# Kernel optimization log

Measured on AMD Instinct MI355X. Metric: run time of the kernel, lower is better.

Reference implementation:

```python
import jax, jax.numpy as jnp
import numpy as np

D_MODEL = 1024
N_HEADS = 16
D_HEAD = D_MODEL // N_HEADS


def setup_inputs() -> dict:
    key = jax.random.key(0)
    kx, kq, kk, kv, ko = jax.random.split(key, 5)
    s = 1.0 / np.sqrt(D_MODEL)
    return {
        "x": jax.random.normal(kx, (2, 2048, D_MODEL), dtype=jnp.float32),
        "Wq": jax.random.normal(kq, (D_MODEL, D_MODEL), dtype=jnp.float32) * s,
        "Wk": jax.random.normal(kk, (D_MODEL, D_MODEL), dtype=jnp.float32) * s,
        "Wv": jax.random.normal(kv, (D_MODEL, D_MODEL), dtype=jnp.float32) * s,
        "Wo": jax.random.normal(ko, (D_MODEL, D_MODEL), dtype=jnp.float32) * s,
    }


def reference(x, Wq, Wk, Wv, Wo):
    B, T, _ = x.shape
    def split_heads(t):  # [B,T,D] -> [B,H,T,d]
        return t.reshape(B, T, N_HEADS, D_HEAD).transpose(0, 2, 1, 3)
    q = split_heads(x @ Wq)
    k = split_heads(x @ Wk)
    v = split_heads(x @ Wv)
    scale = jnp.asarray(D_HEAD, x.dtype) ** -0.5
    att = jnp.einsum("bhqd,bhkd->bhqk", q, k) * scale
    mask = jnp.tril(jnp.ones((T, T), dtype=x.dtype))  # 1 on/below diag
    att = att + (1.0 - mask)[None, None] * jnp.asarray(-1e9, x.dtype)
    w = jax.nn.softmax(att, axis=-1)
    y = jnp.einsum("bhqk,bhkd->bhqd", w, v)
    y = y.transpose(0, 2, 1, 3).reshape(B, T, D_MODEL)
    return y @ Wo
```

## Files before the change

### kernel.cpp

```cpp
#include <hip/hip_runtime.h>

#define DM 1024
#define NH 16
#define TT 2048
#define BB 2
#define NTOK (BB*TT)
#define DQKV 3072

typedef __attribute__((ext_vector_type(8))) short bf16x8;
typedef __attribute__((ext_vector_type(4))) float f32x4;
typedef __attribute__((ext_vector_type(4))) int  int4v;

static __device__ __forceinline__ short f2b(float f) {
  union { float f; unsigned u; } v; v.f = f;
  unsigned r = v.u + 0x7FFFu + ((v.u >> 16) & 1u);
  return (short)(r >> 16);
}

__global__ __launch_bounds__(256) void k_convert(const float* __restrict__ in,
                                                 short* __restrict__ out, int n) {
  int i = (blockIdx.x * 256 + threadIdx.x) * 8;
  if (i >= n) return;
  float4 a = *(const float4*)(in + i);
  float4 b = *(const float4*)(in + i + 4);
  bf16x8 o;
  o[0]=f2b(a.x); o[1]=f2b(a.y); o[2]=f2b(a.z); o[3]=f2b(a.w);
  o[4]=f2b(b.x); o[5]=f2b(b.y); o[6]=f2b(b.z); o[7]=f2b(b.w);
  *(bf16x8*)(out + i) = o;
}

__global__ __launch_bounds__(256) void k_transpose_w4(const float* __restrict__ Wq,
                                                      const float* __restrict__ Wk,
                                                      const float* __restrict__ Wv,
                                                      const float* __restrict__ Wo,
                                                      short* __restrict__ WqkvT,
                                                      short* __restrict__ WoT) {
  __shared__ short t[64][72];
  const int z = blockIdx.z;
  const float* W = (z == 0) ? Wq : (z == 1) ? Wk : (z == 2) ? Wv : Wo;
  short* Wt = (z < 3) ? WqkvT : WoT;
  const int row0 = (z < 3) ? z * 1024 : 0;
  int tid = threadIdx.x;
  int n0 = blockIdx.x * 64, k0 = blockIdx.y * 64;
  #pragma unroll
  for (int i = 0; i < 4; i++) {
    int id = tid + 256 * i;
    int r = id >> 4;
    int c = id & 15;
    float4 v = *(const float4*)(W + (size_t)(k0 + r) * DM + n0 + c * 4);
    t[c*4+0][r] = f2b(v.x);
    t[c*4+1][r] = f2b(v.y);
    t[c*4+2][r] = f2b(v.z);
    t[c*4+3][r] = f2b(v.w);
  }
  __syncthreads();
  #pragma unroll
  for (int i = 0; i < 2; i++) {
    int id = tid + 256 * i;
    int r = id >> 3;
    int c = id & 7;
    bf16x8 o = *(const bf16x8*)&t[r][c * 8];
    *(bf16x8*)(Wt + (size_t)(row0 + n0 + r) * DM + k0 + c * 8) = o;
  }
}

__global__ __launch_bounds__(256) void k_transpose_v(const short* __restrict__ V,
                                                     short* __restrict__ Vt) {
  __shared__ short t[64][72];
  int tid = threadIdx.x;
  int bh = blockIdx.y;
  int b = bh >> 4, h = bh & 15;
  int t0 = blockIdx.x * 64;
  #pragma unroll
  for (int i = 0; i < 2; i++) {
    int id = tid + 256 * i;
    int r = id >> 3;
    int c = id & 7;
    int kp = ((r & 15) << 2) | (r >> 4);
    bf16x8 v = *(const bf16x8*)(V + (size_t)(b * TT + t0 + r) * DQKV + h * 64 + c * 8);
    #pragma unroll
    for (int e = 0; e < 8; e++) t[c * 8 + e][kp] = v[e];
  }
  __syncthreads();
  #pragma unroll
  for (int i = 0; i < 2; i++) {
    int id = tid + 256 * i;
    int r = id >> 3;
    int c = id & 7;
    bf16x8 o = *(const bf16x8*)&t[r][c * 8];
    *(bf16x8*)(Vt + (size_t)(bh * 64 + r) * TT + t0 + c * 8) = o;
  }
}

template<int OUT_BF16, int BN>
__global__ __launch_bounds__(256) void k_gemm_lds(const short* __restrict__ A,
                                                  const short* __restrict__ Bt,
                                                  void* __restrict__ C,
                                                  int M, int N, int K,
                                                  int qcols, float qscale) {
  __shared__ short As[2][128 * 64];
  __shared__ short Bs[2][BN * 64];
  constexpr int NI = BN / 32;
  const int tid = threadIdx.x;
  const int lane = tid & 63, w = tid >> 6;
  const int wm = w >> 1, wn = w & 1;
  const int l15 = lane & 15, g = lane >> 4;
  const int nx = N / BN;
  const int cx = nx >> 3;
  const int bid = blockIdx.x;
  const int xcd = bid & 7, k_ = bid >> 3;
  const int bx = xcd * cx + (k_ % cx), by = k_ / cx;
  const int m0 = by * 128, n0 = bx * BN;
  const int srow = lane >> 3;
  const int scol = ((lane & 7) ^ srow) * 8;
  const int rsw = l15 & 7;

  auto stage = [&](int buf, int k0) {
    #pragma unroll
    for (int i = 0; i < 4; i++) {
      int rbase = w * 32 + i * 8;
      __builtin_amdgcn_global_load_lds(
        (const __attribute__((address_space(1))) void*)(A + (size_t)(m0 + rbase + srow) * K + k0 + scol),
        (__attribute__((address_space(3))) void*)&As[buf][rbase * 64],
        16, 0, 0);
    }
    #pragma unroll
    for (int i = 0; i < BN / 32; i++) {
      int rbase = w * (BN / 4) + i * 8;
      __builtin_amdgcn_global_load_lds(
        (const __attribute__((address_space(1))) void*)(Bt + (size_t)(n0 + rbase + srow) * K + k0 + scol),
        (__attribute__((address_space(3))) void*)&Bs[buf][rbase * 64],
        16, 0, 0);
    }
  };

  f32x4 acc[4][NI] = {};
  stage(0, 0);
  __syncthreads();
  const int nt = K / 64;
  for (int t = 0; t < nt; t++) {
    const int cur = t & 1;
    if (t + 1 < nt) stage(cur ^ 1, (t + 1) * 64);
    #pragma unroll
    for (int kk = 0; kk < 64; kk += 32) {
      bf16x8 af[4], bfr[NI];
      #pragma unroll
      for (int mi = 0; mi < 4; mi++)
        af[mi] = *(const bf16x8*)&As[cur][(wm * 64 + mi * 16 + l15) * 64 + ((((kk >> 3) + g) ^ rsw) << 3)];
      #pragma unroll
      for (int ni = 0; ni < NI; ni++)
        bfr[ni] = *(const bf16x8*)&Bs[cur][(wn * (BN / 2) + ni * 16 + l15) * 64 + ((((kk >> 3) + g) ^ rsw) << 3)];
      #pragma unroll
      for (int mi = 0; mi < 4; mi++)
        #pragma unroll
        for (int ni = 0; ni < NI; ni++)
          acc[mi][ni] = __builtin_amdgcn_mfma_f32_16x16x32_bf16(af[mi], bfr[ni], acc[mi][ni], 0, 0, 0);
    }
    __syncthreads();
  }

  if (OUT_BF16) {
    short* Cs = &As[0][0];
    #pragma unroll
    for (int mi = 0; mi < 4; mi++) {
      #pragma unroll
      for (int ni = 0; ni < NI; ni++) {
        #pragma unroll
        for (int j = 0; j < 4; j++) {
          int row = wm * 64 + mi * 16 + g * 4 + j;
          int col = wn * (BN / 2) + ni * 16 + l15;
          float v = acc[mi][ni][j];
          if (n0 + col < qcols) v *= qscale;
          Cs[row * BN + col] = f2b(v);
        }
      }
    }
    __syncthreads();
    constexpr int UNITS = 128 * BN / 8;
    #pragma unroll
    for (int u = tid; u < UNITS; u += 256) {
      int row = u / (BN / 8), ch = u % (BN / 8);
      bf16x8 vv = *(const bf16x8*)&Cs[row * BN + ch * 8];
      *(bf16x8*)((short*)C + (size_t)(m0 + row) * N + n0 + ch * 8) = vv;
    }
  } else {
    #pragma unroll
    for (int mi = 0; mi < 4; mi++) {
      #pragma unroll
      for (int ni = 0; ni < NI; ni++) {
        #pragma unroll
        for (int j = 0; j < 4; j++) {
          int row = m0 + wm * 64 + mi * 16 + g * 4 + j;
          int col = n0 + wn * (BN / 2) + ni * 16 + l15;
          ((float*)C)[(size_t)row * N + col] = acc[mi][ni][j];
        }
      }
    }
  }
}

__global__ __launch_bounds__(256) void k_attn(const short* __restrict__ Qkv,
                                              const short* __restrict__ Vt,
                                              short* __restrict__ Y) {
  __shared__ short Ks[2][64 * 64];
  __shared__ short Vs[2][64 * 64];
  __shared__ short Ps[4][16 * 64];
  const int tid = threadIdx.x;
  const int lane = tid & 63, w = tid >> 6;
  const int l15 = lane & 15, g = lane >> 4;
  const int bx = blockIdx.x;
  const int xcd = bx & 7, idx = bx >> 3;
  const int bh = xcd * 4 + (idx & 3);
  const int qt = 31 - (idx >> 2);
  const int b = bh >> 4, h = bh & 15;
  const int q0 = qt * 64;
  const int nkt = qt + 1;
  const short* Qb = Qkv;
  const short* Kb = Qkv + DM;
  short* PsW = Ps[w];
  const int rsw = l15 & 7;

  const bf16x8 vones = {0x3F80, 0x3F80, 0x3F80, 0x3F80, 0x3F80, 0x3F80, 0x3F80, 0x3F80};

  auto stage = [&](int buf, int kt) {
    #pragma unroll
    for (int i = 0; i < 2; i++) {
      int id = tid + 256 * i;
      int r = id >> 3;
      int cl = (id ^ r) & 7;
      __builtin_amdgcn_global_load_lds(
        (const __attribute__((address_space(1))) void*)(Kb + (size_t)(b * TT + kt * 64 + r) * DQKV + h * 64 + cl * 8),
        (__attribute__((address_space(3))) void*)&Ks[buf][(w * 64 + 256 * i) * 8],
        16, 0, 0);
      __builtin_amdgcn_global_load_lds(
        (const __attribute__((address_space(1))) void*)(Vt + (size_t)(bh * 64 + r) * TT + kt * 64 + cl * 8),
        (__attribute__((address_space(3))) void*)&Vs[buf][(w * 64 + 256 * i) * 8],
        16, 0, 0);
    }
  };

  bf16x8 aq[2];
  #pragma unroll
  for (int kc = 0; kc < 2; kc++)
    aq[kc] = *(const bf16x8*)(Qb + (size_t)(b * TT + q0 + w * 16 + l15) * DQKV + h * 64 + kc * 32 + 8 * g);

  f32x4 accO[4] = {};
  f32x4 accL = {};
  float m2[4];
  #pragma unroll
  for (int j = 0; j < 4; j++) m2[j] = -1e30f;

  stage(0, 0);
  __syncthreads();

  for (int kt = 0; kt < nkt; kt++) {
    const int cur = kt & 1;
    if (kt + 1 < nkt) stage(cur ^ 1, kt + 1);

    f32x4 accS[4] = {};
    __builtin_amdgcn_s_setprio(1);
    #pragma unroll
    for (int n = 0; n < 4; n++) {
      #pragma unroll
      for (int kc = 0; kc < 2; kc++) {
        bf16x8 bk = *(const bf16x8*)&Ks[cur][(n * 16 + l15) * 64 + (((kc * 4 + g) ^ rsw) << 3)];
        accS[n] = __builtin_amdgcn_mfma_f32_16x16x32_bf16(aq[kc], bk, accS[n], 0, 0, 0);
      }
    }
    __builtin_amdgcn_s_setprio(0);

    float tmaxp[4];
    #pragma unroll
    for (int j = 0; j < 4; j++) tmaxp[j] = -1e30f;
    const int qbase = q0 + w * 16 + g * 4;
    if (kt == qt) {
      #pragma unroll
      for (int n = 0; n < 4; n++) {
        int key = kt * 64 + n * 16 + l15;
        #pragma unroll
        for (int j = 0; j < 4; j++) {
          float s = accS[n][j];
          if (key > qbase + j) s = -1e30f;
          accS[n][j] = s;
          tmaxp[j] = fmaxf(tmaxp[j], s);
        }
      }
    } else {
      #pragma unroll
      for (int n = 0; n < 4; n++)
        #pragma unroll
        for (int j = 0; j < 4; j++)
          tmaxp[j] = fmaxf(tmaxp[j], accS[n][j]);
    }

    float dmax = fmaxf(fmaxf(tmaxp[0] - m2[0], tmaxp[1] - m2[1]),
                       fmaxf(tmaxp[2] - m2[2], tmaxp[3] - m2[3]));
    if (!__all(dmax <= 8.0f)) {
      #pragma unroll
      for (int j = 0; j < 4; j++) {
        float t = tmaxp[j];
        #pragma unroll
        for (int off = 1; off < 16; off <<= 1)
          t = fmaxf(t, __shfl_xor(t, off));
        float mnew = fmaxf(m2[j], t);
        float al = exp2f(m2[j] - mnew);
        m2[j] = mnew;
        accL[j] *= al;
        #pragma unroll
        for (int n2 = 0; n2 < 4; n2++) accO[n2][j] *= al;
      }
    }

    #pragma unroll
    for (int j = 0; j < 4; j++) {
      const int row = g * 4 + j;
      union { float f; unsigned u; } c0, c1, c2, c3;
      c0.f = exp2f(accS[0][j] - m2[j]);
      c1.f = exp2f(accS[1][j] - m2[j]);
      c2.f = exp2f(accS[2][j] - m2[j]);
      c3.f = exp2f(accS[3][j] - m2[j]);
      int2 pk;
      pk.x = (int)((c0.u >> 16) | (c1.u & 0xFFFF0000u));
      pk.y = (int)((c2.u >> 16) | (c3.u & 0xFFFF0000u));
      const int c8 = l15 ^ ((row & 7) << 1);
      *(int2*)&PsW[row * 64 + (c8 << 2)] = pk;
    }

    __builtin_amdgcn_s_setprio(1);
    #pragma unroll
    for (int kc = 0; kc < 2; kc++) {
      bf16x8 pa = *(const bf16x8*)&PsW[l15 * 64 + (((kc * 4 + g) ^ rsw) << 3)];
      #pragma unroll
      for (int n2 = 0; n2 < 4; n2++) {
        bf16x8 vb = *(const bf16x8*)&Vs[cur][(n2 * 16 + l15) * 64 + (((kc * 4 + g) ^ rsw) << 3)];
        accO[n2] = __builtin_amdgcn_mfma_f32_16x16x32_bf16(pa, vb, accO[n2], 0, 0, 0);
      }
      accL = __builtin_amdgcn_mfma_f32_16x16x32_bf16(pa, vones, accL, 0, 0, 0);
    }
    __builtin_amdgcn_s_setprio(0);

    __syncthreads();
  }

  float inv[4];
  #pragma unroll
  for (int j = 0; j < 4; j++) inv[j] = 1.0f / accL[j];
  #pragma unroll
  for (int n2 = 0; n2 < 4; n2++) {
    #pragma unroll
    for (int j = 0; j < 4; j++) {
      float v = accO[n2][j] * inv[j];
      PsW[(g * 4 + j) * 64 + n2 * 16 + l15] = f2b(v);
    }
  }
  const int orow = b * TT + q0 + w * 16;
  #pragma unroll
  for (int i = 0; i < 2; i++) {
    int unit = lane + 64 * i;
    int row = unit >> 3, ch = unit & 7;
    bf16x8 vv = *(const bf16x8*)&PsW[row * 64 + ch * 8];
    *(bf16x8*)(Y + (size_t)(orow + row) * DM + h * 64 + ch * 8) = vv;
  }
}

extern "C" void kernel_launch(void* const* d_in, const int* in_sizes, int n_in,
                              void* d_out, int out_size, void* d_ws, size_t ws_size,
                              hipStream_t stream) {
  const float* x  = (const float*)d_in[0];
  const float* Wq = (const float*)d_in[1];
  const float* Wk = (const float*)d_in[2];
  const float* Wv = (const float*)d_in[3];
  const float* Wo = (const float*)d_in[4];
  float* out = (float*)d_out;

  char* ws = (char*)d_ws;
  size_t off = 0;
  auto alloc = [&](size_t bytes) {
    char* p = ws + off;
    off += (bytes + 255) & ~(size_t)255;
    return p;
  };
  short* xb    = (short*)alloc((size_t)NTOK * DM * 2);
  short* WqkvT = (short*)alloc((size_t)DQKV * DM * 2);
  short* WoT   = (short*)alloc((size_t)DM * DM * 2);
  short* Qkv   = (short*)alloc((size_t)NTOK * DQKV * 2);
  short* Vt    = (short*)alloc((size_t)NTOK * DM * 2);
  short* Yb    = xb;
  if (off > ws_size) return;

  k_convert<<<(NTOK * DM) / (256 * 8), 256, 0, stream>>>(x, xb, NTOK * DM);
  k_transpose_w4<<<dim3(DM / 64, DM / 64, 4), 256, 0, stream>>>(Wq, Wk, Wv, Wo, WqkvT, WoT);

  const float QSC = 0.125f * 1.44269504088896f;
  k_gemm_lds<1, 64><<<dim3((DQKV / 64) * (NTOK / 128)), 256, 0, stream>>>(xb, WqkvT, Qkv, NTOK, DQKV, DM, DM, QSC);

  k_transpose_v<<<dim3(TT / 64, BB * NH), 256, 0, stream>>>(Qkv + 2048, Vt);
  k_attn<<<dim3(1024), 256, 0, stream>>>(Qkv, Vt, Yb);

  k_gemm_lds<0, 64><<<dim3((DM / 64) * (NTOK / 128)), 256, 0, stream>>>(Yb, WoT, out, NTOK, DM, DM, 0, 1.0f);
}
```

Measured before the change: 110.9 us.

## Compute S transposed so P feeds PV MFMA from registers, dropping LDS

```diff
diff --git a/kernel.cpp b/kernel.cpp
--- a/kernel.cpp
+++ b/kernel.cpp
@@ -76,7 +76,8 @@
     int id = tid + 256 * i;
     int r = id >> 3;
     int c = id & 7;
-    int kp = ((r & 15) << 2) | (r >> 4);
+    int n = r >> 4;
+    int kp = ((n >> 1) << 5) | (((r >> 2) & 3) << 3) | ((n & 1) << 2) | (r & 3);
     bf16x8 v = *(const bf16x8*)(V + (size_t)(b * TT + t0 + r) * DQKV + h * 64 + c * 8);
     #pragma unroll
     for (int e = 0; e < 8; e++) t[c * 8 + e][kp] = v[e];
@@ -204,7 +205,6 @@
                                               short* __restrict__ Y) {
   __shared__ short Ks[2][64 * 64];
   __shared__ short Vs[2][64 * 64];
-  __shared__ short Ps[4][16 * 64];
   const int tid = threadIdx.x;
   const int lane = tid & 63, w = tid >> 6;
   const int l15 = lane & 15, g = lane >> 4;
@@ -217,7 +217,6 @@
   const int nkt = qt + 1;
   const short* Qb = Qkv;
   const short* Kb = Qkv + DM;
-  short* PsW = Ps[w];
   const int rsw = l15 & 7;
 
   const bf16x8 vones = {0x3F80, 0x3F80, 0x3F80, 0x3F80, 0x3F80, 0x3F80, 0x3F80, 0x3F80};
@@ -246,9 +245,7 @@
 
   f32x4 accO[4] = {};
   f32x4 accL = {};
-  float m2[4];
-  #pragma unroll
-  for (int j = 0; j < 4; j++) m2[j] = -1e30f;
+  float m2 = -1e30f;
 
   stage(0, 0);
   __syncthreads();
@@ -264,72 +261,65 @@
       #pragma unroll
       for (int kc = 0; kc < 2; kc++) {
         bf16x8 bk = *(const bf16x8*)&Ks[cur][(n * 16 + l15) * 64 + (((kc * 4 + g) ^ rsw) << 3)];
-        accS[n] = __builtin_amdgcn_mfma_f32_16x16x32_bf16(aq[kc], bk, accS[n], 0, 0, 0);
+        accS[n] = __builtin_amdgcn_mfma_f32_16x16x32_bf16(bk, aq[kc], accS[n], 0, 0, 0);
       }
     }
     __builtin_amdgcn_s_setprio(0);
 
-    float tmaxp[4];
-    #pragma unroll
-    for (int j = 0; j < 4; j++) tmaxp[j] = -1e30f;
-    const int qbase = q0 + w * 16 + g * 4;
+    const int qg = q0 + w * 16 + l15;
     if (kt == qt) {
       #pragma unroll
       for (int n = 0; n < 4; n++) {
-        int key = kt * 64 + n * 16 + l15;
         #pragma unroll
         for (int j = 0; j < 4; j++) {
-          float s = accS[n][j];
-          if (key > qbase + j) s = -1e30f;
-          accS[n][j] = s;
-          tmaxp[j] = fmaxf(tmaxp[j], s);
+          int key = kt * 64 + n * 16 + g * 4 + j;
+          if (key > qg) accS[n][j] = -1e30f;
         }
       }
-    } else {
-      #pragma unroll
-      for (int n = 0; n < 4; n++)
-        #pragma unroll
-        for (int j = 0; j < 4; j++)
-          tmaxp[j] = fmaxf(tmaxp[j], accS[n][j]);
-    }
-
-    float dmax = fmaxf(fmaxf(tmaxp[0] - m2[0], tmaxp[1] - m2[1]),
-                       fmaxf(tmaxp[2] - m2[2], tmaxp[3] - m2[3]));
-    if (!__all(dmax <= 8.0f)) {
+    }
+    float tmax = -1e30f;
+    #pragma unroll
+    for (int n = 0; n < 4; n++)
+      #pragma unroll
+      for (int j = 0; j < 4; j++)
+        tmax = fmaxf(tmax, accS[n][j]);
+
+    if (!__all(tmax - m2 <= 8.0f)) {
+      float t1 = fmaxf(tmax, __shfl_xor(tmax, 16));
+      float full = fmaxf(t1, __shfl_xor(t1, 32));
+      float mnew = fmaxf(m2, full);
+      float al = exp2f(m2 - mnew);
+      m2 = mnew;
+      float alr[4];
+      #pragma unroll
+      for (int j = 0; j < 4; j++) alr[j] = __shfl(al, g * 4 + j);
+      #pragma unroll
+      for (int j = 0; j < 4; j++) accL[j] *= alr[j];
+      #pragma unroll
+      for (int n2 = 0; n2 < 4; n2++)
+        #pragma unroll
+        for (int j = 0; j < 4; j++) accO[n2][j] *= alr[j];
+    }
+
+    unsigned cu[4][4];
+    #pragma unroll
+    for (int n = 0; n < 4; n++)
       #pragma unroll
       for (int j = 0; j < 4; j++) {
-        float t = tmaxp[j];
-        #pragma unroll
-        for (int off = 1; off < 16; off <<= 1)
-          t = fmaxf(t, __shfl_xor(t, off));
-        float mnew = fmaxf(m2[j], t);
-        float al = exp2f(m2[j] - mnew);
-        m2[j] = mnew;
-        accL[j] *= al;
-        #pragma unroll
-        for (int n2 = 0; n2 < 4; n2++) accO[n2][j] *= al;
-      }
-    }
-
-    #pragma unroll
-    for (int j = 0; j < 4; j++) {
-      const int row = g * 4 + j;
-      union { float f; unsigned u; } c0, c1, c2, c3;
-      c0.f = exp2f(accS[0][j] - m2[j]);
-      c1.f = exp2f(accS[1][j] - m2[j]);
-      c2.f = exp2f(accS[2][j] - m2[j]);
-      c3.f = exp2f(accS[3][j] - m2[j]);
-      int2 pk;
-      pk.x = (int)((c0.u >> 16) | (c1.u & 0xFFFF0000u));
-      pk.y = (int)((c2.u >> 16) | (c3.u & 0xFFFF0000u));
-      const int c8 = l15 ^ ((row & 7) << 1);
-      *(int2*)&PsW[row * 64 + (c8 << 2)] = pk;
-    }
+        union { float f; unsigned u; } cv;
+        cv.f = exp2f(accS[n][j] - m2);
+        cu[n][j] = cv.u;
+      }
 
     __builtin_amdgcn_s_setprio(1);
     #pragma unroll
     for (int kc = 0; kc < 2; kc++) {
-      bf16x8 pa = *(const bf16x8*)&PsW[l15 * 64 + (((kc * 4 + g) ^ rsw) << 3)];
+      union { int4v i; bf16x8 h; } pu;
+      pu.i[0] = (int)((cu[2*kc+0][0] >> 16) | (cu[2*kc+0][1] & 0xFFFF0000u));
+      pu.i[1] = (int)((cu[2*kc+0][2] >> 16) | (cu[2*kc+0][3] & 0xFFFF0000u));
+      pu.i[2] = (int)((cu[2*kc+1][0] >> 16) | (cu[2*kc+1][1] & 0xFFFF0000u));
+      pu.i[3] = (int)((cu[2*kc+1][2] >> 16) | (cu[2*kc+1][3] & 0xFFFF0000u));
+      bf16x8 pa = pu.h;
       #pragma unroll
       for (int n2 = 0; n2 < 4; n2++) {
         bf16x8 vb = *(const bf16x8*)&Vs[cur][(n2 * 16 + l15) * 64 + (((kc * 4 + g) ^ rsw) << 3)];
@@ -345,12 +335,13 @@
   float inv[4];
   #pragma unroll
   for (int j = 0; j < 4; j++) inv[j] = 1.0f / accL[j];
+  short* Ys = &Ks[0][w * 1024];
   #pragma unroll
   for (int n2 = 0; n2 < 4; n2++) {
     #pragma unroll
     for (int j = 0; j < 4; j++) {
       float v = accO[n2][j] * inv[j];
-      PsW[(g * 4 + j) * 64 + n2 * 16 + l15] = f2b(v);
+      Ys[(g * 4 + j) * 64 + n2 * 16 + l15] = f2b(v);
     }
   }
   const int orow = b * TT + q0 + w * 16;
@@ -358,7 +349,7 @@
   for (int i = 0; i < 2; i++) {
     int unit = lane + 64 * i;
     int row = unit >> 3, ch = unit & 7;
-    bf16x8 vv = *(const bf16x8*)&PsW[row * 64 + ch * 8];
+    bf16x8 vv = *(const bf16x8*)&Ys[row * 64 + ch * 8];
     *(bf16x8*)(Y + (size_t)(orow + row) * DM + h * 64 + ch * 8) = vv;
   }
 }
```

Result: slower. 114.4 us (+3.2%).
